# Performance work log

Hardware: AMD Instinct MI355X
Metric: run time of the kernel (lower is better)

The kernel has to match this reference:

```python
import jax, jax.numpy as jnp
import numpy as np

H = 256  # hidden_dim
NH = 4   # num_heads
HD = H // NH  # head dim


def setup_inputs() -> dict:
    key = jax.random.key(0)
    ks = jax.random.split(key, 12)
    B, TD, ID = 65536, 512, 512
    s_t = 1.0 / np.sqrt(TD)
    s_h = 1.0 / np.sqrt(H)
    s_f = 1.0 / np.sqrt(2 * H)
    return {
        "text_features": jax.random.normal(ks[0], (B, TD), jnp.float32),
        "image_features": jax.random.normal(ks[1], (B, ID), jnp.float32),
        "W_text": jax.random.uniform(ks[2], (H, TD), jnp.float32, -s_t, s_t),
        "b_text": jax.random.uniform(ks[3], (H,), jnp.float32, -s_t, s_t),
        "W_img": jax.random.uniform(ks[4], (H, ID), jnp.float32, -s_t, s_t),
        "b_img": jax.random.uniform(ks[5], (H,), jnp.float32, -s_t, s_t),
        "in_proj_w": jax.random.normal(ks[6], (3 * H, H), jnp.float32) * s_h,  # xavier-ish
        "in_proj_b": jnp.zeros((3 * H,), jnp.float32),
        "out_proj_w": jax.random.uniform(ks[7], (H, H), jnp.float32, -s_h, s_h),
        "out_proj_b": jnp.zeros((H,), jnp.float32),
        "W_fuse": jax.random.uniform(ks[8], (H, 2 * H), jnp.float32, -s_f, s_f),
        "b_fuse": jax.random.uniform(ks[9], (H,), jnp.float32, -s_f, s_f),
    }


def _mha_seq1(q_in, kv_in, in_proj_w, in_proj_b, out_proj_w, out_proj_b):
    """nn.MultiheadAttention with query seq_len=1 and kv seq_len=1 (eval mode).
    q_in, kv_in: [B, H]. Softmax over the single key is identically 1."""
    Wq, Wk, Wv = jnp.split(in_proj_w, 3, axis=0)
    bq, bk, bv = jnp.split(in_proj_b, 3, axis=0)
    q = (q_in @ Wq.T + bq).reshape(-1, NH, HD)   # [B, nh, hd]
    k = (kv_in @ Wk.T + bk).reshape(-1, NH, HD)
    v = (kv_in @ Wv.T + bv).reshape(-1, NH, HD)
    scores = jnp.einsum("bnd,bnd->bn", q, k) / np.sqrt(HD)  # [B, nh], one key
    attn = jax.nn.softmax(scores[..., None], axis=-1)       # == 1 exactly
    out = (attn * v).reshape(-1, H)                          # concat heads
    return out @ out_proj_w.T + out_proj_b


def reference(text_features, image_features, W_text, b_text, W_img, b_img,
              in_proj_w, in_proj_b, out_proj_w, out_proj_b, W_fuse, b_fuse):
    tp = text_features @ W_text.T + b_text      # [B, H]
    ip = image_features @ W_img.T + b_img       # [B, H]
    text_att = _mha_seq1(tp, ip, in_proj_w, in_proj_b, out_proj_w, out_proj_b)
    img_att = _mha_seq1(ip, tp, in_proj_w, in_proj_b, out_proj_w, out_proj_b)
    fused = jnp.concatenate([text_att, img_att], axis=1)  # [B, 2H]
    return jax.nn.relu(fused @ W_fuse.T + b_fuse)          # dropout = eval no-op
```

## Files before the change

### kernel.cpp

```cpp
#include <hip/hip_runtime.h>
#include <hip/hip_bf16.h>

typedef __attribute__((ext_vector_type(4))) float floatx4;
typedef __attribute__((ext_vector_type(2))) float floatx2;
typedef __attribute__((ext_vector_type(8))) __bf16 bf16x8;
typedef __attribute__((ext_vector_type(8))) unsigned short ushortx8;

__device__ __forceinline__ unsigned short f2bf(float x) {
    union { float f; unsigned u; } v; v.f = x;
    unsigned r = v.u + 0x7fffu + ((v.u >> 16) & 1u);
    return (unsigned short)(r >> 16);
}

__device__ __forceinline__ bf16x8 as_bf(ushortx8 v) {
    union { ushortx8 u; bf16x8 b; } x; x.u = v; return x.b;
}

__device__ __forceinline__ ushortx8 cvt8u(floatx4 lo, floatx4 hi) {
    union { ushortx8 v; __hip_bfloat162 h[4]; } u;
    float2 p;
    p.x = lo.x; p.y = lo.y; u.h[0] = __float22bfloat162_rn(p);
    p.x = lo.z; p.y = lo.w; u.h[1] = __float22bfloat162_rn(p);
    p.x = hi.x; p.y = hi.y; u.h[2] = __float22bfloat162_rn(p);
    p.x = hi.z; p.y = hi.w; u.h[3] = __float22bfloat162_rn(p);
    return u.v;
}

__global__ void k1_tree(const float* __restrict__ W_fuse, const float* __restrict__ OP,
                        const float* __restrict__ ipw, const float* __restrict__ ipb,
                        const float* __restrict__ W_img, const float* __restrict__ W_text,
                        const float* __restrict__ opb, const float* __restrict__ b_img,
                        const float* __restrict__ b_text,
                        float* __restrict__ U0, float* __restrict__ U1,
                        float* __restrict__ Vimg, float* __restrict__ Vtxt,
                        float* __restrict__ vb_img, float* __restrict__ vb_txt,
                        float* __restrict__ cvec) {
    const int bid = blockIdx.x;
    const int t = threadIdx.x;
    const float* Wv = ipw + 512 * 256;
    if (bid == 96) {
        if (t < 256) {
            float a0 = opb[t], a1 = 0.f, a2 = 0.f;
            const float* oprow = OP + t * 256;
            const float* wvrow = Wv + t * 256;
            #pragma unroll 4
            for (int k = 0; k < 256; ++k) {
                a0 = fmaf(oprow[k], ipb[512 + k], a0);
                a1 = fmaf(wvrow[k], b_img[k], a1);
                a2 = fmaf(wvrow[k], b_text[k], a2);
            }
            cvec[t] = a0; vb_img[t] = a1; vb_txt[t] = a2;
        }
        return;
    }
    const float *A, *B; float* C; int lda, ldb, ldc, aoff, tm, tn;
    if (bid < 32) {
        int h = bid >> 4, tt = bid & 15;
        A = W_fuse; lda = 512; aoff = h * 256;
        B = OP; ldb = 256; C = h ? U1 : U0; ldc = 256;
        tm = tt >> 2; tn = tt & 3;
    } else {
        int b2 = bid - 32; int h = b2 >> 5; int tt = b2 & 31;
        A = Wv; lda = 256; aoff = 0;
        B = h ? W_text : W_img; ldb = 512; C = h ? Vtxt : Vimg; ldc = 512;
        tm = tt >> 3; tn = tt & 7;
    }
    __shared__ float As[16][68];
    __shared__ float Bs[16][68];
    const int arow = t >> 3, ak = (t & 7) * 2;
    const int brow = t >> 5, bc = (t & 31) * 2;
    const int ty = t >> 4, tx = t & 15;
    float acc[2][4] = {};
    for (int k0 = 0; k0 < 256; k0 += 16) {
        floatx2 av = *(const floatx2*)(A + (size_t)(tm * 64 + arow) * lda + aoff + k0 + ak);
        floatx2 bv = *(const floatx2*)(B + (size_t)(k0 + brow) * ldb + tn * 64 + bc);
        __syncthreads();
        As[ak + 0][arow] = av.x;
        As[ak + 1][arow] = av.y;
        *(floatx2*)&Bs[brow][bc] = bv;
        __syncthreads();
        #pragma unroll
        for (int kk = 0; kk < 16; ++kk) {
            floatx2 a = *(const floatx2*)&As[kk][ty * 2];
            floatx4 b = *(const floatx4*)&Bs[kk][tx * 4];
            acc[0][0] = fmaf(a.x, b.x, acc[0][0]); acc[0][1] = fmaf(a.x, b.y, acc[0][1]);
            acc[0][2] = fmaf(a.x, b.z, acc[0][2]); acc[0][3] = fmaf(a.x, b.w, acc[0][3]);
            acc[1][0] = fmaf(a.y, b.x, acc[1][0]); acc[1][1] = fmaf(a.y, b.y, acc[1][1]);
            acc[1][2] = fmaf(a.y, b.z, acc[1][2]); acc[1][3] = fmaf(a.y, b.w, acc[1][3]);
        }
    }
    #pragma unroll
    for (int i = 0; i < 2; ++i) {
        floatx4 o; o.x = acc[i][0]; o.y = acc[i][1]; o.z = acc[i][2]; o.w = acc[i][3];
        *(floatx4*)(C + (size_t)(tm * 64 + ty * 2 + i) * ldc + tn * 64 + tx * 4) = o;
    }
}

__global__ void k2_A(const float* __restrict__ U0, const float* __restrict__ U1,
                     const float* __restrict__ Vimg, const float* __restrict__ Vtxt,
                     const float* __restrict__ W_fuse, const float* __restrict__ b_fuse,
                     const float* __restrict__ vb_img, const float* __restrict__ vb_txt,
                     const float* __restrict__ cvec,
                     unsigned short* __restrict__ Wt, float* __restrict__ b_total) {
    const int bid = blockIdx.x;
    const int t = threadIdx.x;
    if (bid == 64) {
        if (t < 256) {
            float acc = b_fuse[t];
            const float* u0 = U0 + t * 256;
            const float* u1 = U1 + t * 256;
            const float* wf = W_fuse + t * 512;
            #pragma unroll 4
            for (int j = 0; j < 256; ++j) {
                acc = fmaf(u0[j], vb_img[j], acc);
                acc = fmaf(u1[j], vb_txt[j], acc);
                acc = fmaf(wf[j] + wf[j + 256], cvec[j], acc);
            }
            b_total[t] = acc;
        }
        return;
    }
    const int h = bid >> 5, tt = bid & 31;
    const float* A = h ? U1 : U0;
    const float* B = h ? Vtxt : Vimg;
    const int tm = tt >> 3, tn = tt & 7;
    __shared__ float As[16][68];
    __shared__ float Bs[16][68];
    const int arow = t >> 3, ak = (t & 7) * 2;
    const int brow = t >> 5, bc = (t & 31) * 2;
    const int n_l = t >> 3, oct = t & 7;
    float acc[8] = {};
    for (int k0 = 0; k0 < 256; k0 += 16) {
        floatx2 av = *(const floatx2*)(A + (size_t)(tm * 64 + arow) * 256 + k0 + ak);
        floatx2 bv = *(const floatx2*)(B + (size_t)(k0 + brow) * 512 + tn * 64 + bc);
        __syncthreads();
        As[ak + 0][arow] = av.x;
        As[ak + 1][arow] = av.y;
        *(floatx2*)&Bs[brow][bc] = bv;
        __syncthreads();
        #pragma unroll
        for (int kk = 0; kk < 16; ++kk) {
            float u = As[kk][n_l];
            floatx4 v0 = *(const floatx4*)&Bs[kk][oct * 8];
            floatx4 v1 = *(const floatx4*)&Bs[kk][oct * 8 + 4];
            acc[0] = fmaf(u, v0.x, acc[0]); acc[1] = fmaf(u, v0.y, acc[1]);
            acc[2] = fmaf(u, v0.z, acc[2]); acc[3] = fmaf(u, v0.w, acc[3]);
            acc[4] = fmaf(u, v1.x, acc[4]); acc[5] = fmaf(u, v1.y, acc[5]);
            acc[6] = fmaf(u, v1.z, acc[6]); acc[7] = fmaf(u, v1.w, acc[7]);
        }
    }
    const int n = tm * 64 + n_l;
    const int kg = h * 512 + tn * 64 + oct * 8;
    const int kq = kg >> 5, q = (kg >> 3) & 3;
    const int nt = n >> 4, nl = n & 15;
    union { ushortx8 v; unsigned short s[8]; } o;
    #pragma unroll
    for (int j = 0; j < 8; ++j) o.s[j] = f2bf(acc[j]);
    *(ushortx8*)&Wt[(size_t)((nt * 32 + kq) * 64 + q * 16 + nl) * 8] = o.v;
}

__global__ __launch_bounds__(256, 4)
void fused_gemm(const float* __restrict__ Ximg, const float* __restrict__ Xtxt,
                const unsigned short* __restrict__ Wt,
                const float* __restrict__ b_total, float* __restrict__ out) {
    __shared__ unsigned short lds[2][32 * 264];
    const int t = threadIdx.x, lane = t & 63, w = t >> 6;
    const int ml = lane & 15, q = lane >> 4;
    const size_t rowbase = (size_t)blockIdx.x * 32;
    const int sr = t >> 3;
    const int sc = (t & 7) * 32;

    floatx4 acc[2][4];
    #pragma unroll
    for (int mi = 0; mi < 2; ++mi)
        #pragma unroll
        for (int ni = 0; ni < 4; ++ni) acc[mi][ni] = (floatx4){0.f, 0.f, 0.f, 0.f};

    floatx4 lr[8];

    auto load_regs = [&](int s) {
        const float* X = (s < 2) ? Ximg : Xtxt;
        const float* gp = X + (rowbase + sr) * 512 + (s & 1) * 256 + sc;
        #pragma unroll
        for (int i = 0; i < 8; ++i) lr[i] = *(const floatx4*)(gp + i * 4);
    };
    auto write_stage = [&](int b) {
        unsigned short* lp = &lds[b][sr * 264 + sc];
        #pragma unroll
        for (int j = 0; j < 4; ++j)
            *(ushortx8*)(lp + j * 8) = cvt8u(lr[2 * j], lr[2 * j + 1]);
    };
    auto compute = [&](int s, int b) {
        #pragma unroll
        for (int kqi = 0; kqi < 8; ++kqi) {
            const int kq = s * 8 + kqi;
            bf16x8 af[2];
            #pragma unroll
            for (int mi = 0; mi < 2; ++mi) {
                const unsigned short* ap = &lds[b][(mi * 16 + ml) * 264 + kqi * 32 + q * 8];
                af[mi] = as_bf(*(const ushortx8*)ap);
            }
            #pragma unroll
            for (int ni = 0; ni < 4; ++ni) {
                ushortx8 bv = *(const ushortx8*)(Wt + (size_t)(((w * 4 + ni) * 32 + kq) * 64 + lane) * 8);
                #pragma unroll
                for (int mi = 0; mi < 2; ++mi)
                    acc[mi][ni] = __builtin_amdgcn_mfma_f32_16x16x32_bf16(af[mi], as_bf(bv), acc[mi][ni], 0, 0, 0);
            }
        }
    };

    load_regs(0);
    write_stage(0);
    __syncthreads();
    #pragma unroll
    for (int s = 0; s < 4; ++s) {
        if (s < 3) load_regs(s + 1);
        compute(s, s & 1);
        if (s < 3) {
            write_stage((s + 1) & 1);
            __syncthreads();
        }
    }

    #pragma unroll
    for (int ni = 0; ni < 4; ++ni) {
        const int col = w * 64 + ni * 16 + ml;
        const float bias = b_total[col];
        #pragma unroll
        for (int mi = 0; mi < 2; ++mi) {
            const size_t r0 = rowbase + mi * 16 + q * 4;
            #pragma unroll
            for (int e = 0; e < 4; ++e) {
                float v = acc[mi][ni][e] + bias;
                out[(r0 + e) * 256 + col] = fmaxf(v, 0.f);
            }
        }
    }
}

extern "C" void kernel_launch(void* const* d_in, const int* in_sizes, int n_in,
                              void* d_out, int out_size, void* d_ws, size_t ws_size,
                              hipStream_t stream) {
    const float* text       = (const float*)d_in[0];
    const float* image      = (const float*)d_in[1];
    const float* W_text     = (const float*)d_in[2];
    const float* b_text     = (const float*)d_in[3];
    const float* W_img      = (const float*)d_in[4];
    const float* b_img      = (const float*)d_in[5];
    const float* in_proj_w  = (const float*)d_in[6];
    const float* in_proj_b  = (const float*)d_in[7];
    const float* out_proj_w = (const float*)d_in[8];
    const float* out_proj_b = (const float*)d_in[9];
    const float* W_fuse     = (const float*)d_in[10];
    const float* b_fuse     = (const float*)d_in[11];
    float* out = (float*)d_out;

    float* ws      = (float*)d_ws;
    float* U0      = ws;
    float* U1      = ws + 65536;
    float* Vimg    = ws + 131072;
    float* Vtxt    = ws + 262144;
    float* vb_img  = ws + 393216;
    float* vb_txt  = ws + 393472;
    float* cvec    = ws + 393728;
    float* b_total = ws + 393984;
    unsigned short* Wt = (unsigned short*)(ws + 394240);

    k1_tree<<<dim3(97), dim3(512), 0, stream>>>(W_fuse, out_proj_w, in_proj_w, in_proj_b,
                                                W_img, W_text, out_proj_b, b_img, b_text,
                                                U0, U1, Vimg, Vtxt, vb_img, vb_txt, cvec);
    k2_A<<<dim3(65), dim3(512), 0, stream>>>(U0, U1, Vimg, Vtxt, W_fuse, b_fuse,
                                             vb_img, vb_txt, cvec, Wt, b_total);
    fused_gemm<<<dim3(2048), dim3(256), 0, stream>>>(image, text, Wt, b_total, out);
}
```

Baseline: 398.7 us.

## Retile weight-folding GEMMs into smaller 32x32 tiles across more blocks

The two small prologue kernels that fold the projection weights now use 32x32 output tiles, 256 threads and 128-wide K chunks with vectorized shared-memory staging. They launch 385 and 257 blocks instead of 97 and 65, which spreads the weight-folding work over many more CUs. The k2 epilogue writes 4-element bf16 pieces into the packed Wt layout. The main fused_gemm launch bound also drops its min-blocks hint from 4 to 3, which may give the compiler more registers but can lower occupancy.

After: 390.9 us. About the same (-1.9%).

```diff
diff --git a/kernel.cpp b/kernel.cpp
--- a/kernel.cpp
+++ b/kernel.cpp
@@ -5,6 +5,7 @@
 typedef __attribute__((ext_vector_type(2))) float floatx2;
 typedef __attribute__((ext_vector_type(8))) __bf16 bf16x8;
 typedef __attribute__((ext_vector_type(8))) unsigned short ushortx8;
+typedef __attribute__((ext_vector_type(4))) unsigned short ushortx4;
 
 __device__ __forceinline__ unsigned short f2bf(float x) {
     union { float f; unsigned u; } v; v.f = x;
@@ -38,62 +39,61 @@
     const int bid = blockIdx.x;
     const int t = threadIdx.x;
     const float* Wv = ipw + 512 * 256;
-    if (bid == 96) {
-        if (t < 256) {
-            float a0 = opb[t], a1 = 0.f, a2 = 0.f;
-            const float* oprow = OP + t * 256;
-            const float* wvrow = Wv + t * 256;
-            #pragma unroll 4
-            for (int k = 0; k < 256; ++k) {
-                a0 = fmaf(oprow[k], ipb[512 + k], a0);
-                a1 = fmaf(wvrow[k], b_img[k], a1);
-                a2 = fmaf(wvrow[k], b_text[k], a2);
-            }
-            cvec[t] = a0; vb_img[t] = a1; vb_txt[t] = a2;
-        }
+    if (bid == 384) {
+        float a0 = opb[t], a1 = 0.f, a2 = 0.f;
+        const float* oprow = OP + t * 256;
+        const float* wvrow = Wv + t * 256;
+        #pragma unroll 4
+        for (int k = 0; k < 256; ++k) {
+            a0 = fmaf(oprow[k], ipb[512 + k], a0);
+            a1 = fmaf(wvrow[k], b_img[k], a1);
+            a2 = fmaf(wvrow[k], b_text[k], a2);
+        }
+        cvec[t] = a0; vb_img[t] = a1; vb_txt[t] = a2;
         return;
     }
-    const float *A, *B; float* C; int lda, ldb, ldc, aoff, tm, tn;
-    if (bid < 32) {
-        int h = bid >> 4, tt = bid & 15;
+    const float *A, *B; float* C; int lda, ldb, ldc, aoff, row0, col0;
+    if (bid < 128) {
+        int h = bid >> 6, tt = bid & 63;
         A = W_fuse; lda = 512; aoff = h * 256;
         B = OP; ldb = 256; C = h ? U1 : U0; ldc = 256;
-        tm = tt >> 2; tn = tt & 3;
+        row0 = (tt >> 3) * 32; col0 = (tt & 7) * 32;
     } else {
-        int b2 = bid - 32; int h = b2 >> 5; int tt = b2 & 31;
+        int b2 = bid - 128; int h = b2 >> 7; int tt = b2 & 127;
         A = Wv; lda = 256; aoff = 0;
         B = h ? W_text : W_img; ldb = 512; C = h ? Vtxt : Vimg; ldc = 512;
-        tm = tt >> 3; tn = tt & 7;
-    }
-    __shared__ float As[16][68];
-    __shared__ float Bs[16][68];
-    const int arow = t >> 3, ak = (t & 7) * 2;
-    const int brow = t >> 5, bc = (t & 31) * 2;
-    const int ty = t >> 4, tx = t & 15;
-    float acc[2][4] = {};
-    for (int k0 = 0; k0 < 256; k0 += 16) {
-        floatx2 av = *(const floatx2*)(A + (size_t)(tm * 64 + arow) * lda + aoff + k0 + ak);
-        floatx2 bv = *(const floatx2*)(B + (size_t)(k0 + brow) * ldb + tn * 64 + bc);
-        __syncthreads();
-        As[ak + 0][arow] = av.x;
-        As[ak + 1][arow] = av.y;
-        *(floatx2*)&Bs[brow][bc] = bv;
-        __syncthreads();
-        #pragma unroll
-        for (int kk = 0; kk < 16; ++kk) {
-            floatx2 a = *(const floatx2*)&As[kk][ty * 2];
-            floatx4 b = *(const floatx4*)&Bs[kk][tx * 4];
-            acc[0][0] = fmaf(a.x, b.x, acc[0][0]); acc[0][1] = fmaf(a.x, b.y, acc[0][1]);
-            acc[0][2] = fmaf(a.x, b.z, acc[0][2]); acc[0][3] = fmaf(a.x, b.w, acc[0][3]);
-            acc[1][0] = fmaf(a.y, b.x, acc[1][0]); acc[1][1] = fmaf(a.y, b.y, acc[1][1]);
-            acc[1][2] = fmaf(a.y, b.z, acc[1][2]); acc[1][3] = fmaf(a.y, b.w, acc[1][3]);
-        }
-    }
-    #pragma unroll
-    for (int i = 0; i < 2; ++i) {
-        floatx4 o; o.x = acc[i][0]; o.y = acc[i][1]; o.z = acc[i][2]; o.w = acc[i][3];
-        *(floatx4*)(C + (size_t)(tm * 64 + ty * 2 + i) * ldc + tn * 64 + tx * 4) = o;
-    }
+        row0 = (tt >> 4) * 32; col0 = (tt & 15) * 32;
+    }
+    __shared__ float As[32][132];
+    __shared__ float Bs[128][40];
+    const int ar = t >> 3, ac = (t & 7) * 16;
+    const int bk = t >> 1, bc = (t & 1) * 16;
+    const int r = t >> 3, c4 = (t & 7) * 4;
+    float acc0 = 0.f, acc1 = 0.f, acc2 = 0.f, acc3 = 0.f;
+    for (int k0 = 0; k0 < 256; k0 += 128) {
+        floatx4 at[4], bt[4];
+        const float* ap = A + (size_t)(row0 + ar) * lda + aoff + k0 + ac;
+        const float* bp = B + (size_t)(k0 + bk) * ldb + col0 + bc;
+        #pragma unroll
+        for (int i = 0; i < 4; ++i) at[i] = *(const floatx4*)(ap + i * 4);
+        #pragma unroll
+        for (int i = 0; i < 4; ++i) bt[i] = *(const floatx4*)(bp + i * 4);
+        __syncthreads();
+        #pragma unroll
+        for (int i = 0; i < 4; ++i) *(floatx4*)&As[ar][ac + i * 4] = at[i];
+        #pragma unroll
+        for (int i = 0; i < 4; ++i) *(floatx4*)&Bs[bk][bc + i * 4] = bt[i];
+        __syncthreads();
+        #pragma unroll 4
+        for (int k = 0; k < 128; ++k) {
+            float a = As[r][k];
+            floatx4 b = *(const floatx4*)&Bs[k][c4];
+            acc0 = fmaf(a, b.x, acc0); acc1 = fmaf(a, b.y, acc1);
+            acc2 = fmaf(a, b.z, acc2); acc3 = fmaf(a, b.w, acc3);
+        }
+    }
+    floatx4 o; o.x = acc0; o.y = acc1; o.z = acc2; o.w = acc3;
+    *(floatx4*)(C + (size_t)(row0 + r) * ldc + col0 + c4) = o;
 }
 
 __global__ void k2_A(const float* __restrict__ U0, const float* __restrict__ U1,
@@ -104,62 +104,62 @@
                      unsigned short* __restrict__ Wt, float* __restrict__ b_total) {
     const int bid = blockIdx.x;
     const int t = threadIdx.x;
-    if (bid == 64) {
-        if (t < 256) {
-            float acc = b_fuse[t];
-            const float* u0 = U0 + t * 256;
-            const float* u1 = U1 + t * 256;
-            const float* wf = W_fuse + t * 512;
-            #pragma unroll 4
-            for (int j = 0; j < 256; ++j) {
-                acc = fmaf(u0[j], vb_img[j], acc);
-                acc = fmaf(u1[j], vb_txt[j], acc);
-                acc = fmaf(wf[j] + wf[j + 256], cvec[j], acc);
-            }
-            b_total[t] = acc;
-        }
+    if (bid == 256) {
+        float acc = b_fuse[t];
+        const float* u0 = U0 + t * 256;
+        const float* u1 = U1 + t * 256;
+        const float* wf = W_fuse + t * 512;
+        #pragma unroll 4
+        for (int j = 0; j < 256; ++j) {
+            acc = fmaf(u0[j], vb_img[j], acc);
+            acc = fmaf(u1[j], vb_txt[j], acc);
+            acc = fmaf(wf[j] + wf[j + 256], cvec[j], acc);
+        }
+        b_total[t] = acc;
         return;
     }
-    const int h = bid >> 5, tt = bid & 31;
+    const int h = bid >> 7, tt = bid & 127;
     const float* A = h ? U1 : U0;
     const float* B = h ? Vtxt : Vimg;
-    const int tm = tt >> 3, tn = tt & 7;
-    __shared__ float As[16][68];
-    __shared__ float Bs[16][68];
-    const int arow = t >> 3, ak = (t & 7) * 2;
-    const int brow = t >> 5, bc = (t & 31) * 2;
-    const int n_l = t >> 3, oct = t & 7;
-    float acc[8] = {};
-    for (int k0 = 0; k0 < 256; k0 += 16) {
-        floatx2 av = *(const floatx2*)(A + (size_t)(tm * 64 + arow) * 256 + k0 + ak);
-        floatx2 bv = *(const floatx2*)(B + (size_t)(k0 + brow) * 512 + tn * 64 + bc);
-        __syncthreads();
-        As[ak + 0][arow] = av.x;
-        As[ak + 1][arow] = av.y;
-        *(floatx2*)&Bs[brow][bc] = bv;
-        __syncthreads();
-        #pragma unroll
-        for (int kk = 0; kk < 16; ++kk) {
-            float u = As[kk][n_l];
-            floatx4 v0 = *(const floatx4*)&Bs[kk][oct * 8];
-            floatx4 v1 = *(const floatx4*)&Bs[kk][oct * 8 + 4];
-            acc[0] = fmaf(u, v0.x, acc[0]); acc[1] = fmaf(u, v0.y, acc[1]);
-            acc[2] = fmaf(u, v0.z, acc[2]); acc[3] = fmaf(u, v0.w, acc[3]);
-            acc[4] = fmaf(u, v1.x, acc[4]); acc[5] = fmaf(u, v1.y, acc[5]);
-            acc[6] = fmaf(u, v1.z, acc[6]); acc[7] = fmaf(u, v1.w, acc[7]);
-        }
-    }
-    const int n = tm * 64 + n_l;
-    const int kg = h * 512 + tn * 64 + oct * 8;
-    const int kq = kg >> 5, q = (kg >> 3) & 3;
+    const int row0 = (tt >> 4) * 32, col0 = (tt & 15) * 32;
+    __shared__ float As[32][132];
+    __shared__ float Bs[128][40];
+    const int ar = t >> 3, ac = (t & 7) * 16;
+    const int bk = t >> 1, bc = (t & 1) * 16;
+    const int r = t >> 3, c4 = (t & 7) * 4;
+    float acc0 = 0.f, acc1 = 0.f, acc2 = 0.f, acc3 = 0.f;
+    for (int k0 = 0; k0 < 256; k0 += 128) {
+        floatx4 at[4], bt[4];
+        const float* ap = A + (size_t)(row0 + ar) * 256 + k0 + ac;
+        const float* bp = B + (size_t)(k0 + bk) * 512 + col0 + bc;
+        #pragma unroll
+        for (int i = 0; i < 4; ++i) at[i] = *(const floatx4*)(ap + i * 4);
+        #pragma unroll
+        for (int i = 0; i < 4; ++i) bt[i] = *(const floatx4*)(bp + i * 4);
+        __syncthreads();
+        #pragma unroll
+        for (int i = 0; i < 4; ++i) *(floatx4*)&As[ar][ac + i * 4] = at[i];
+        #pragma unroll
+        for (int i = 0; i < 4; ++i) *(floatx4*)&Bs[bk][bc + i * 4] = bt[i];
+        __syncthreads();
+        #pragma unroll 4
+        for (int k = 0; k < 128; ++k) {
+            float a = As[r][k];
+            floatx4 b = *(const floatx4*)&Bs[k][c4];
+            acc0 = fmaf(a, b.x, acc0); acc1 = fmaf(a, b.y, acc1);
+            acc2 = fmaf(a, b.z, acc2); acc3 = fmaf(a, b.w, acc3);
+        }
+    }
+    const int n = row0 + r;
+    const int kgg = h * 512 + col0 + c4;
+    const int kq = kgg >> 5, q = (kgg >> 3) & 3, e0 = kgg & 7;
     const int nt = n >> 4, nl = n & 15;
-    union { ushortx8 v; unsigned short s[8]; } o;
-    #pragma unroll
-    for (int j = 0; j < 8; ++j) o.s[j] = f2bf(acc[j]);
-    *(ushortx8*)&Wt[(size_t)((nt * 32 + kq) * 64 + q * 16 + nl) * 8] = o.v;
-}
-
-__global__ __launch_bounds__(256, 4)
+    union { ushortx4 v; unsigned short s[4]; } o;
+    o.s[0] = f2bf(acc0); o.s[1] = f2bf(acc1); o.s[2] = f2bf(acc2); o.s[3] = f2bf(acc3);
+    *(ushortx4*)&Wt[(size_t)((nt * 32 + kq) * 64 + q * 16 + nl) * 8 + e0] = o.v;
+}
+
+__global__ __launch_bounds__(256, 3)
 void fused_gemm(const float* __restrict__ Ximg, const float* __restrict__ Xtxt,
                 const unsigned short* __restrict__ Wt,
                 const float* __restrict__ b_total, float* __restrict__ out) {
@@ -267,10 +267,10 @@
     float* b_total = ws + 393984;
     unsigned short* Wt = (unsigned short*)(ws + 394240);
 
-    k1_tree<<<dim3(97), dim3(512), 0, stream>>>(W_fuse, out_proj_w, in_proj_w, in_proj_b,
-                                                W_img, W_text, out_proj_b, b_img, b_text,
-                                                U0, U1, Vimg, Vtxt, vb_img, vb_txt, cvec);
-    k2_A<<<dim3(65), dim3(512), 0, stream>>>(U0, U1, Vimg, Vtxt, W_fuse, b_fuse,
-                                             vb_img, vb_txt, cvec, Wt, b_total);
+    k1_tree<<<dim3(385), dim3(256), 0, stream>>>(W_fuse, out_proj_w, in_proj_w, in_proj_b,
+                                                 W_img, W_text, out_proj_b, b_img, b_text,
+                                                 U0, U1, Vimg, Vtxt, vb_img, vb_txt, cvec);
+    k2_A<<<dim3(257), dim3(256), 0, stream>>>(U0, U1, Vimg, Vtxt, W_fuse, b_fuse,
+                                              vb_img, vb_txt, cvec, Wt, b_total);
     fused_gemm<<<dim3(2048), dim3(256), 0, stream>>>(image, text, Wt, b_total, out);
 }
```
